# Optimization experiments

Hardware: AMD Instinct MI355X
Metric: run time of the kernel (lower is better)

## Reference

```python
import jax, jax.numpy as jnp
import numpy as np

N_NODES = 100000


def _segment_mean(h, src, dst, n_nodes):
    # copy_u: gather source features along edges, then mean-reduce per dst node
    msg = h[src]                                             # [E, D]
    s = jax.ops.segment_sum(msg, dst, num_segments=n_nodes)  # [N, D]
    cnt = jax.ops.segment_sum(jnp.ones((src.shape[0],), h.dtype), dst,
                              num_segments=n_nodes)          # [N]
    return s / jnp.maximum(cnt, 1.0)[:, None]


def setup_inputs() -> dict:
    key = jax.random.key(0)
    k1, k2, k3, k4, k5 = jax.random.split(key, 5)
    in_feats, n_hidden, n_classes = 128, 128, 64
    n_edges = 1600000
    features = jax.random.normal(k1, (N_NODES, in_feats), dtype=jnp.float32)
    W1 = jax.random.normal(k2, (in_feats, n_hidden), dtype=jnp.float32) * (1.0 / np.sqrt(in_feats))
    b1 = jnp.zeros((n_hidden,), jnp.float32)
    W2 = jax.random.normal(k3, (n_hidden, n_classes), dtype=jnp.float32) * (1.0 / np.sqrt(n_hidden))
    b2 = jnp.zeros((n_classes,), jnp.float32)
    src = jax.random.randint(k4, (n_edges,), 0, N_NODES, dtype=jnp.int64)
    dst = jax.random.randint(k5, (n_edges,), 0, N_NODES, dtype=jnp.int64)
    return {"features": features, "W1": W1, "b1": b1, "W2": W2, "b2": b2,
            "src": src, "dst": dst}


def reference(features, W1, b1, W2, b2, src, dst):
    # Layer 0: mean aggregation -> Linear -> relu  (dropout p=0.0 is identity)
    h = _segment_mean(features, src, dst, N_NODES)
    h = jax.nn.relu(h @ W1 + b1)
    # Layer 1: mean aggregation -> Linear (no activation on output layer)
    h = _segment_mean(h, src, dst, N_NODES)
    h = h @ W2 + b2
    return h
```

## Files before the change

kernel.cpp:

```cpp
#include <hip/hip_runtime.h>

#define N_NODES 100000
#define D 128
#define NE 1600000
#define C_OUT 64
#define NB 391
#define SENT 100000
#define P2B 256
#define P2E 6250
#define SEGSTRIDE 6400

typedef _Float16 half8 __attribute__((ext_vector_type(8)));
typedef float floatx4 __attribute__((ext_vector_type(4)));


__device__ inline half8 shfl_xor_h8(half8 v, int mask) {
    union { half8 h; int i[4]; } u;
    u.h = v;
    u.i[0] = __shfl_xor(u.i[0], mask);
    u.i[1] = __shfl_xor(u.i[1], mask);
    u.i[2] = __shfl_xor(u.i[2], mask);
    u.i[3] = __shfl_xor(u.i[3], mask);
    return u.h;
}

__device__ inline void pack_one(const float* W, _Float16* Wp, int tid, int N) {
    int l = tid & 63, p = tid >> 6;
    int nt = p >> 2, kc = p & 3;
    int quad = l >> 4, c = l & 15;
    int n = nt * 16 + c;
    half8 h;
    #pragma unroll
    for (int j = 0; j < 8; ++j) {
        int k = kc * 32 + quad * 8 + j;
        h[j] = (_Float16)W[k * N + n];
    }
    *(half8*)(Wp + (size_t)p * 512 + l * 8) = h;
}

__global__ __launch_bounds__(1024) void k1_p2_setup(const int* __restrict__ src,
                                                    const int* __restrict__ dst,
                                                    unsigned* __restrict__ gwords,
                                                    int* __restrict__ ofsg,
                                                    const float* __restrict__ W1,
                                                    const float* __restrict__ W2,
                                                    _Float16* __restrict__ wp1,
                                                    _Float16* __restrict__ wp2,
                                                    int* __restrict__ t1s,
                                                    int* __restrict__ t2s) {
    if (blockIdx.x >= P2B) {
        const int blk = blockIdx.x - P2B;
        const int t = threadIdx.x;
        if (t < 256) {
            if (blk < 8) {
                pack_one(W1, wp1, blk * 256 + t, 128);
            } else if (blk < 12) {
                pack_one(W2, wp2, (blk - 8) * 256 + t, 64);
            } else {
                if (t < 64) t1s[t] = 0;
                else if (t < 96) t2s[t - 64] = 0;
            }
        }
        return;
    }

    __shared__ unsigned ebuf[P2E];
    __shared__ int hist[NB];
    __shared__ int ofs[NB + 1];
    __shared__ int cur[NB];
    __shared__ int wsum[8];
    const int t = threadIdx.x;
    const int base = blockIdx.x * P2E;

    for (int i = t; i < NB; i += 1024) hist[i] = 0;
    __syncthreads();

    unsigned w[7];
    int bk[7];
    #pragma unroll
    for (int r = 0; r < 7; ++r) {
        const int j = r * 1024 + t;
        if (j < P2E) {
            const int e = base + j;
            const int d = dst[e];
            w[r] = ((unsigned)(d & 255) << 20) | (unsigned)src[e];
            bk[r] = d >> 8;
            atomicAdd(&hist[bk[r]], 1);
        } else {
            bk[r] = -1;
        }
    }
    __syncthreads();

    int v = 0, incl = 0;
    if (t < 512) { v = (t < NB) ? hist[t] : 0; incl = v; }
    #pragma unroll
    for (int d = 1; d < 64; d <<= 1) {
        int y = __shfl_up(incl, d);
        if ((t & 63) >= d) incl += y;
    }
    if (t < 512 && (t & 63) == 63) wsum[t >> 6] = incl;
    __syncthreads();
    if (t < NB) {
        int ex = incl - v;
        const int wv = t >> 6;
        for (int j = 0; j < wv; ++j) ex += wsum[j];
        ofs[t] = ex;
        cur[t] = ex;
    }
    if (t == 0) ofs[NB] = P2E;
    __syncthreads();

    #pragma unroll
    for (int r = 0; r < 7; ++r) {
        if (bk[r] >= 0) {
            const int slot = atomicAdd(&cur[bk[r]], 1);
            ebuf[slot] = w[r];
        }
    }
    __syncthreads();

    unsigned* gout = gwords + (size_t)blockIdx.x * SEGSTRIDE;
    for (int i = t; i < P2E; i += 1024) gout[i] = ebuf[i];
    int* oout = ofsg + blockIdx.x * (NB + 1);
    for (int i = t; i < NB + 1; i += 1024) oout[i] = ofs[i];
}

__global__ __launch_bounds__(256) void k2_p3_gemm1(const unsigned* __restrict__ gwords,
                                                   const int* __restrict__ ofsg,
                                                   int* __restrict__ ptrp,
                                                   int* __restrict__ pcnt,
                                                   float* __restrict__ inv,
                                                   int* __restrict__ csr,
                                                   const float* __restrict__ A,
                                                   const _Float16* __restrict__ Wp,
                                                   _Float16* __restrict__ outh) {
    __shared__ __align__(16) char smem[40960];
    const int t = threadIdx.x;

    if (blockIdx.x < NB) {
        unsigned* wbuf = (unsigned*)smem;
        int* sa   = (int*)(smem + 32768);
        int* so   = (int*)(smem + 33792);
        int* lcnt = (int*)(smem + 34816);
        int* lofs = (int*)(smem + 35840);
        int* ws4  = (int*)(smem + 36864);
        const int b = blockIdx.x;
        const int lane = t & 63, wave = t >> 6;

        const int* row = ofsg + t * (NB + 1);
        const int a0 = row[b];
        const int len = row[b + 1] - a0;
        sa[t] = a0;
        lcnt[t] = 0;
        int sv = a0;
        #pragma unroll
        for (int m2 = 1; m2 < 64; m2 <<= 1) sv += __shfl_xor(sv, m2);
        if (lane == 0) ws4[wave] = sv;
        __syncthreads();
        const int pad_base = (ws4[0] + ws4[1] + ws4[2] + ws4[3]) + 1792 * b;
        __syncthreads();

        int incl = len;
        #pragma unroll
        for (int d = 1; d < 64; d <<= 1) {
            int y = __shfl_up(incl, d);
            if (lane >= d) incl += y;
        }
        if (lane == 63) ws4[wave] = incl;
        __syncthreads();
        int off = incl - len;
        for (int j = 0; j < wave; ++j) off += ws4[j];
        so[t] = off;
        const int tot = min(ws4[0] + ws4[1] + ws4[2] + ws4[3], 8192);
        __syncthreads();

        {
            const int per = (tot + 255) >> 8;
            const int lo = t * per;
            const int hi = min(lo + per, tot);
            if (lo < hi) {
                int l = 0, r = P2B;
                while (r - l > 1) {
                    const int m = (l + r) >> 1;
                    if (so[m] <= lo) l = m; else r = m;
                }
                int sg = l;
                #pragma unroll 4
                for (int i = lo; i < hi; ++i) {
                    while (sg + 1 < P2B && so[sg + 1] <= i) ++sg;
                    const unsigned w = gwords[(size_t)sg * SEGSTRIDE + sa[sg] + (i - so[sg])];
                    wbuf[i] = w;
                    atomicAdd(&lcnt[(w >> 20) & 255], 1);
                }
            }
        }
        __syncthreads();

        const int v = lcnt[t];
        const int pc = (v + 7) & ~7;
        int incl2 = pc;
        #pragma unroll
        for (int d = 1; d < 64; d <<= 1) {
            int y = __shfl_up(incl2, d);
            if (lane >= d) incl2 += y;
        }
        __syncthreads();
        if (lane == 63) ws4[wave] = incl2;
        __syncthreads();
        int ex = incl2 - pc;
        for (int j = 0; j < wave; ++j) ex += ws4[j];

        const int node = b * 256 + t;
        if (node < N_NODES) {
            ptrp[node] = pad_base + ex;
            pcnt[node] = pc;
            inv[node] = 1.0f / fmaxf((float)v, 1.0f);
        }
        for (int j = v; j < pc; ++j) csr[pad_base + ex + j] = SENT;

        __syncthreads();
        lofs[t] = ex;
        __syncthreads();
        for (int i = t; i < tot; i += 256) {
            const unsigned w = wbuf[i];
            const int pos = atomicAdd(&lofs[(w >> 20) & 255], 1);
            csr[pad_base + pos] = (int)(w & 0xFFFFF);
        }
        return;
    }

    _Float16* Wl = (_Float16*)smem;
    _Float16* Al = (_Float16*)(smem + 32768);
    {
        const floatx4* s4 = (const floatx4*)Wp;
        floatx4* d4 = (floatx4*)Wl;
        #pragma unroll
        for (int i = 0; i < 8; ++i) d4[t + 256 * i] = s4[t + 256 * i];
    }
    const int lane = t & 63;
    const int wave = t >> 6;
    const int row0 = (blockIdx.x - NB) * 128;

    floatx4 acc[8][2];
    #pragma unroll
    for (int mt = 0; mt < 8; ++mt)
        #pragma unroll
        for (int nt = 0; nt < 2; ++nt) acc[mt][nt] = (floatx4)0.0f;

    for (int kc = 0; kc < 4; ++kc) {
        __syncthreads();
        #pragma unroll
        for (int rep = 0; rep < 2; ++rep) {
            int p = rep * 256 + t;
            int r = p >> 2, quad = p & 3;
            int row = row0 + r;
            if (row > N_NODES - 1) row = N_NODES - 1;
            const float4 x0 = *(const float4*)(A + (size_t)row * D + kc * 32 + quad * 8);
            const float4 x1 = *(const float4*)(A + (size_t)row * D + kc * 32 + quad * 8 + 4);
            half8 h;
            h[0] = (_Float16)x0.x; h[1] = (_Float16)x0.y;
            h[2] = (_Float16)x0.z; h[3] = (_Float16)x0.w;
            h[4] = (_Float16)x1.x; h[5] = (_Float16)x1.y;
            h[6] = (_Float16)x1.z; h[7] = (_Float16)x1.w;
            int mt = r >> 4, m = r & 15;
            *(half8*)(Al + mt * 512 + (quad * 16 + m) * 8) = h;
        }
        __syncthreads();
        const half8* Af = (const half8*)Al;
        const half8* Bf = (const half8*)Wl;
        half8 b0 = Bf[((wave * 2 + 0) * 4 + kc) * 64 + lane];
        half8 b1 = Bf[((wave * 2 + 1) * 4 + kc) * 64 + lane];
        #pragma unroll
        for (int mt = 0; mt < 8; ++mt) {
            half8 a = Af[mt * 64 + lane];
            acc[mt][0] = __builtin_amdgcn_mfma_f32_16x16x32_f16(a, b0, acc[mt][0], 0, 0, 0);
            acc[mt][1] = __builtin_amdgcn_mfma_f32_16x16x32_f16(a, b1, acc[mt][1], 0, 0, 0);
        }
    }

    const int quad = lane >> 4, cl = lane & 15;
    #pragma unroll
    for (int mt = 0; mt < 8; ++mt)
        #pragma unroll
        for (int nt = 0; nt < 2; ++nt) {
            int col = wave * 32 + nt * 16 + cl;
            #pragma unroll
            for (int i = 0; i < 4; ++i) {
                int row = row0 + mt * 16 + quad * 4 + i;
                if (row < N_NODES)
                    outh[(size_t)row * D + col] = (_Float16)acc[mt][nt][i];
            }
        }
}

__global__ __launch_bounds__(256) void kF_agg_gemm2(const _Float16* __restrict__ f,
                                                    const int* __restrict__ ptrp,
                                                    const int* __restrict__ pcnt,
                                                    const int* __restrict__ csr,
                                                    const float* __restrict__ inv,
                                                    const float* __restrict__ bias,
                                                    const _Float16* __restrict__ Wp,
                                                    _Float16* __restrict__ outh) {
    __shared__ __align__(16) _Float16 Wl[8192];
    __shared__ __align__(16) _Float16 h1t[16 * 136];
    const int t = threadIdx.x;
    {
        const floatx4* s4 = (const floatx4*)Wp;
        floatx4* d4 = (floatx4*)Wl;
        #pragma unroll
        for (int i = 0; i < 4; ++i) d4[t + 256 * i] = s4[t + 256 * i];
    }
    const int wave = t >> 6;
    const int lane = t & 63;
    const int q = lane & 15, hf = lane >> 4;
    const half8* f8 = (const half8*)f;

    for (int it = 0; it < 4; ++it) {
        const int r = wave * 4 + it;
        const int n = blockIdx.x * 16 + r;
        const int begin = ptrp[n];
        const int end = begin + pcnt[n];
        const float iv = inv[n];

        half8 acc0 = {0, 0, 0, 0, 0, 0, 0, 0};
        half8 acc1 = {0, 0, 0, 0, 0, 0, 0, 0};
        for (int base = begin; base < end; base += 64) {
            const int m = min(64, end - base);
            int edge = (lane < m) ? csr[base + lane] : SENT;
            int i = 0;
            for (; i + 16 <= m; i += 16) {
                int s0 = __shfl(edge, i + hf);
                int s1 = __shfl(edge, i + 4 + hf);
                int s2 = __shfl(edge, i + 8 + hf);
                int s3 = __shfl(edge, i + 12 + hf);
                half8 v0 = f8[(size_t)s0 * 16 + q];
                half8 v1 = f8[(size_t)s1 * 16 + q];
                half8 v2 = f8[(size_t)s2 * 16 + q];
                half8 v3 = f8[(size_t)s3 * 16 + q];
                acc0 += v0;
                acc1 += v1;
                acc0 += v2;
                acc1 += v3;
            }
            if (i < m) {
                int s0 = __shfl(edge, i + hf);
                int s1 = __shfl(edge, i + 4 + hf);
                half8 v0 = f8[(size_t)s0 * 16 + q];
                half8 v1 = f8[(size_t)s1 * 16 + q];
                acc0 += v0;
                acc1 += v1;
            }
        }
        acc0 += acc1;
        acc0 += shfl_xor_h8(acc0, 16);
        acc0 += shfl_xor_h8(acc0, 32);
        if (hf == 0) {
            const float4 b0 = ((const float4*)bias)[q * 2];
            const float4 b1v = ((const float4*)bias)[q * 2 + 1];
            half8 o;
            o[0] = (_Float16)fmaxf((float)acc0[0] * iv + b0.x, 0.f);
            o[1] = (_Float16)fmaxf((float)acc0[1] * iv + b0.y, 0.f);
            o[2] = (_Float16)fmaxf((float)acc0[2] * iv + b0.z, 0.f);
            o[3] = (_Float16)fmaxf((float)acc0[3] * iv + b0.w, 0.f);
            o[4] = (_Float16)fmaxf((float)acc0[4] * iv + b1v.x, 0.f);
            o[5] = (_Float16)fmaxf((float)acc0[5] * iv + b1v.y, 0.f);
            o[6] = (_Float16)fmaxf((float)acc0[6] * iv + b1v.z, 0.f);
            o[7] = (_Float16)fmaxf((float)acc0[7] * iv + b1v.w, 0.f);
            *(half8*)(h1t + r * 136 + q * 8) = o;
        }
    }
    __syncthreads();

    floatx4 acc = (floatx4)0.0f;
    #pragma unroll
    for (int kc = 0; kc < 4; ++kc) {
        half8 a = *(const half8*)(h1t + (lane & 15) * 136 + kc * 32 + (lane >> 4) * 8);
        half8 b = ((const half8*)Wl)[(wave * 4 + kc) * 64 + lane];
        acc = __builtin_amdgcn_mfma_f32_16x16x32_f16(a, b, acc, 0, 0, 0);
    }
    const int quad = lane >> 4, cl = lane & 15;
    const int col = wave * 16 + cl;
    #pragma unroll
    for (int i = 0; i < 4; ++i) {
        const int row = blockIdx.x * 16 + quad * 4 + i;
        outh[(size_t)row * C_OUT + col] = (_Float16)acc[i];
    }
}

__global__ __launch_bounds__(256) void kG_agg64(const _Float16* __restrict__ f,
                                                const int* __restrict__ ptrp,
                                                const int* __restrict__ pcnt,
                                                const int* __restrict__ csr,
                                                const float* __restrict__ inv,
                                                const float* __restrict__ bias,
                                                float* __restrict__ out) {
    const int wave = threadIdx.x >> 6;
    const int lane = threadIdx.x & 63;
    const int q = lane & 7, hf = lane >> 3;
    const int n = blockIdx.x * 4 + wave;
    const int begin = ptrp[n];
    const int end = begin + pcnt[n];
    const float iv = inv[n];
    const half8* f8 = (const half8*)f;

    half8 acc0 = {0, 0, 0, 0, 0, 0, 0, 0};
    half8 acc1 = {0, 0, 0, 0, 0, 0, 0, 0};
    for (int base = begin; base < end; base += 64) {
        const int m = min(64, end - base);
        int edge = (lane < m) ? csr[base + lane] : SENT;
        int i = 0;
        for (; i + 32 <= m; i += 32) {
            int s0 = __shfl(edge, i + hf);
            int s1 = __shfl(edge, i + 8 + hf);
            int s2 = __shfl(edge, i + 16 + hf);
            int s3 = __shfl(edge, i + 24 + hf);
            half8 v0 = f8[(size_t)s0 * 8 + q];
            half8 v1 = f8[(size_t)s1 * 8 + q];
            half8 v2 = f8[(size_t)s2 * 8 + q];
            half8 v3 = f8[(size_t)s3 * 8 + q];
            acc0 += v0;
            acc1 += v1;
            acc0 += v2;
            acc1 += v3;
        }
        if (i + 16 <= m) {
            int s0 = __shfl(edge, i + hf);
            int s1 = __shfl(edge, i + 8 + hf);
            half8 v0 = f8[(size_t)s0 * 8 + q];
            half8 v1 = f8[(size_t)s1 * 8 + q];
            acc0 += v0;
            acc1 += v1;
            i += 16;
        }
        if (i < m) {
            int s = __shfl(edge, i + hf);
            acc0 += f8[(size_t)s * 8 + q];
        }
    }
    acc0 += acc1;
    acc0 += shfl_xor_h8(acc0, 8);
    acc0 += shfl_xor_h8(acc0, 16);
    acc0 += shfl_xor_h8(acc0, 32);
    if (hf == 0) {
        const float4 b0 = ((const float4*)bias)[q * 2];
        const float4 b1 = ((const float4*)bias)[q * 2 + 1];
        float4 o0, o1;
        o0.x = (float)acc0[0] * iv + b0.x;
        o0.y = (float)acc0[1] * iv + b0.y;
        o0.z = (float)acc0[2] * iv + b0.z;
        o0.w = (float)acc0[3] * iv + b0.w;
        o1.x = (float)acc0[4] * iv + b1.x;
        o1.y = (float)acc0[5] * iv + b1.y;
        o1.z = (float)acc0[6] * iv + b1.z;
        o1.w = (float)acc0[7] * iv + b1.w;
        ((float4*)out)[(size_t)n * 16 + q * 2] = o0;
        ((float4*)out)[(size_t)n * 16 + q * 2 + 1] = o1;
    }
}

extern "C" void kernel_launch(void* const* d_in, const int* in_sizes, int n_in,
                              void* d_out, int out_size, void* d_ws, size_t ws_size,
                              hipStream_t stream) {
    const float* features = (const float*)d_in[0];
    const float* W1 = (const float*)d_in[1];
    const float* b1 = (const float*)d_in[2];
    const float* W2 = (const float*)d_in[3];
    const float* b2 = (const float*)d_in[4];
    const int* src = (const int*)d_in[5];
    const int* dst = (const int*)d_in[6];
    float* out = (float*)d_out;

    char* ws = (char*)d_ws;
    int*      ofsg  = (int*)(ws + 512L * 4);
    int*      ptrp  = (int*)(ws + 125952L * 4);
    int*      pcnt  = (int*)(ws + 225952L * 4);
    float*    inv   = (float*)(ws + 325952L * 4);
    int*      csr   = (int*)(ws + 425952L * 4);
    unsigned* gwords= (unsigned*)(ws + 2825952L * 4);
    _Float16* wp1   = (_Float16*)(ws + 4464352L * 4);
    _Float16* wp2   = (_Float16*)(ws + 4472544L * 4);
    _Float16* t1h   = (_Float16*)(ws + 4476640L * 4);
    _Float16* t2h   = (_Float16*)(ws + 17276704L * 4);

    k1_p2_setup<<<P2B + 13, 1024, 0, stream>>>(src, dst, gwords, ofsg, W1, W2, wp1, wp2,
                                               (int*)(t1h + (size_t)SENT * 128),
                                               (int*)(t2h + (size_t)SENT * 64));
    k2_p3_gemm1<<<NB + 782, 256, 0, stream>>>(gwords, ofsg, ptrp, pcnt, inv, csr,
                                              features, wp1, t1h);
    kF_agg_gemm2<<<N_NODES / 16, 256, 0, stream>>>(t1h, ptrp, pcnt, csr, inv, b1, wp2, t2h);
    kG_agg64<<<N_NODES / 4, 256, 0, stream>>>(t2h, ptrp, pcnt, csr, inv, b2, out);
}
```

Before: 228.8 us.

## Move GEMM1 into the first kernel alongside edge bucketing, packing W1 per block

The dense features@W1 GEMM no longer shares a launch with CSR phase 3; it now runs in the first kernel, concurrently with the per-chunk edge bucketing (phase 2). Phase 3 becomes its own small kernel. Each GEMM block packs W1 into fp16 in LDS directly instead of reading a pre-packed copy, and the bucketing blocks are reshaped from 1024 to 256 threads. The goal is to hide the GEMM behind the atomics-bound bucketing pass, at the cost of redundant W1 conversion in every GEMM block and lower per-block parallelism in bucketing.

```diff
diff --git a/kernel.cpp b/kernel.cpp
--- a/kernel.cpp
+++ b/kernel.cpp
@@ -9,6 +9,7 @@
 #define P2B 256
 #define P2E 6250
 #define SEGSTRIDE 6400
+#define GOFF 261
 
 typedef _Float16 half8 __attribute__((ext_vector_type(8)));
 typedef float floatx4 __attribute__((ext_vector_type(4)));
@@ -38,209 +39,110 @@
     *(half8*)(Wp + (size_t)p * 512 + l * 8) = h;
 }
 
-__global__ __launch_bounds__(1024) void k1_p2_setup(const int* __restrict__ src,
-                                                    const int* __restrict__ dst,
-                                                    unsigned* __restrict__ gwords,
-                                                    int* __restrict__ ofsg,
-                                                    const float* __restrict__ W1,
-                                                    const float* __restrict__ W2,
-                                                    _Float16* __restrict__ wp1,
-                                                    _Float16* __restrict__ wp2,
-                                                    int* __restrict__ t1s,
-                                                    int* __restrict__ t2s) {
-    if (blockIdx.x >= P2B) {
-        const int blk = blockIdx.x - P2B;
-        const int t = threadIdx.x;
-        if (t < 256) {
-            if (blk < 8) {
-                pack_one(W1, wp1, blk * 256 + t, 128);
-            } else if (blk < 12) {
-                pack_one(W2, wp2, (blk - 8) * 256 + t, 64);
-            } else {
-                if (t < 64) t1s[t] = 0;
-                else if (t < 96) t2s[t - 64] = 0;
-            }
-        }
-        return;
-    }
-
-    __shared__ unsigned ebuf[P2E];
-    __shared__ int hist[NB];
-    __shared__ int ofs[NB + 1];
-    __shared__ int cur[NB];
-    __shared__ int wsum[8];
+__global__ __launch_bounds__(256) void k1_all(const int* __restrict__ src,
+                                              const int* __restrict__ dst,
+                                              unsigned* __restrict__ gwords,
+                                              int* __restrict__ ofsg,
+                                              const float* __restrict__ W1,
+                                              const float* __restrict__ W2,
+                                              _Float16* __restrict__ wp2,
+                                              int* __restrict__ t1s,
+                                              int* __restrict__ t2s,
+                                              const float* __restrict__ A,
+                                              _Float16* __restrict__ outh) {
+    __shared__ __align__(16) char smem[40960];
     const int t = threadIdx.x;
-    const int base = blockIdx.x * P2E;
-
-    for (int i = t; i < NB; i += 1024) hist[i] = 0;
-    __syncthreads();
-
-    unsigned w[7];
-    int bk[7];
-    #pragma unroll
-    for (int r = 0; r < 7; ++r) {
-        const int j = r * 1024 + t;
-        if (j < P2E) {
+
+    if (blockIdx.x < P2B) {
+        unsigned* ebuf = (unsigned*)smem;
+        int* hist = (int*)(smem + 25088);
+        int* ofs  = (int*)(smem + 27136);
+        int* cur  = (int*)(smem + 28736);
+        int* ws4  = (int*)(smem + 30336);
+        const int base = blockIdx.x * P2E;
+        const int lane = t & 63, wave = t >> 6;
+
+        hist[t] = 0;
+        hist[t + 256] = 0;
+        __syncthreads();
+
+        for (int j = t; j < P2E; j += 256)
+            atomicAdd(&hist[dst[base + j] >> 8], 1);
+        __syncthreads();
+
+        int v0 = hist[t], i0 = v0;
+        #pragma unroll
+        for (int d = 1; d < 64; d <<= 1) {
+            int y = __shfl_up(i0, d);
+            if (lane >= d) i0 += y;
+        }
+        if (lane == 63) ws4[wave] = i0;
+        __syncthreads();
+        int ex0 = i0 - v0;
+        for (int j = 0; j < wave; ++j) ex0 += ws4[j];
+        const int tot0 = ws4[0] + ws4[1] + ws4[2] + ws4[3];
+        __syncthreads();
+        int v1 = hist[256 + t], i1 = v1;
+        #pragma unroll
+        for (int d = 1; d < 64; d <<= 1) {
+            int y = __shfl_up(i1, d);
+            if (lane >= d) i1 += y;
+        }
+        if (lane == 63) ws4[wave] = i1;
+        __syncthreads();
+        int ex1 = i1 - v1 + tot0;
+        for (int j = 0; j < wave; ++j) ex1 += ws4[j];
+        ofs[t] = ex0;
+        cur[t] = ex0;
+        if (256 + t < NB) { ofs[256 + t] = ex1; cur[256 + t] = ex1; }
+        if (t == 0) ofs[NB] = P2E;
+        __syncthreads();
+
+        for (int j = t; j < P2E; j += 256) {
             const int e = base + j;
             const int d = dst[e];
-            w[r] = ((unsigned)(d & 255) << 20) | (unsigned)src[e];
-            bk[r] = d >> 8;
-            atomicAdd(&hist[bk[r]], 1);
+            const unsigned w = ((unsigned)(d & 255) << 20) | (unsigned)src[e];
+            const int slot = atomicAdd(&cur[d >> 8], 1);
+            ebuf[slot] = w;
+        }
+        __syncthreads();
+
+        unsigned* gout = gwords + (size_t)blockIdx.x * SEGSTRIDE;
+        for (int i = t; i < P2E; i += 256) gout[i] = ebuf[i];
+        int* oout = ofsg + blockIdx.x * (NB + 1);
+        for (int i = t; i < NB + 1; i += 256) oout[i] = ofs[i];
+        return;
+    }
+
+    if (blockIdx.x < GOFF) {
+        const int blk = blockIdx.x - P2B;
+        if (blk < 4) {
+            pack_one(W2, wp2, blk * 256 + t, 64);
         } else {
-            bk[r] = -1;
-        }
-    }
-    __syncthreads();
-
-    int v = 0, incl = 0;
-    if (t < 512) { v = (t < NB) ? hist[t] : 0; incl = v; }
-    #pragma unroll
-    for (int d = 1; d < 64; d <<= 1) {
-        int y = __shfl_up(incl, d);
-        if ((t & 63) >= d) incl += y;
-    }
-    if (t < 512 && (t & 63) == 63) wsum[t >> 6] = incl;
-    __syncthreads();
-    if (t < NB) {
-        int ex = incl - v;
-        const int wv = t >> 6;
-        for (int j = 0; j < wv; ++j) ex += wsum[j];
-        ofs[t] = ex;
-        cur[t] = ex;
-    }
-    if (t == 0) ofs[NB] = P2E;
-    __syncthreads();
-
-    #pragma unroll
-    for (int r = 0; r < 7; ++r) {
-        if (bk[r] >= 0) {
-            const int slot = atomicAdd(&cur[bk[r]], 1);
-            ebuf[slot] = w[r];
-        }
-    }
-    __syncthreads();
-
-    unsigned* gout = gwords + (size_t)blockIdx.x * SEGSTRIDE;
-    for (int i = t; i < P2E; i += 1024) gout[i] = ebuf[i];
-    int* oout = ofsg + blockIdx.x * (NB + 1);
-    for (int i = t; i < NB + 1; i += 1024) oout[i] = ofs[i];
-}
-
-__global__ __launch_bounds__(256) void k2_p3_gemm1(const unsigned* __restrict__ gwords,
-                                                   const int* __restrict__ ofsg,
-                                                   int* __restrict__ ptrp,
-                                                   int* __restrict__ pcnt,
-                                                   float* __restrict__ inv,
-                                                   int* __restrict__ csr,
-                                                   const float* __restrict__ A,
-                                                   const _Float16* __restrict__ Wp,
-                                                   _Float16* __restrict__ outh) {
-    __shared__ __align__(16) char smem[40960];
-    const int t = threadIdx.x;
-
-    if (blockIdx.x < NB) {
-        unsigned* wbuf = (unsigned*)smem;
-        int* sa   = (int*)(smem + 32768);
-        int* so   = (int*)(smem + 33792);
-        int* lcnt = (int*)(smem + 34816);
-        int* lofs = (int*)(smem + 35840);
-        int* ws4  = (int*)(smem + 36864);
-        const int b = blockIdx.x;
-        const int lane = t & 63, wave = t >> 6;
-
-        const int* row = ofsg + t * (NB + 1);
-        const int a0 = row[b];
-        const int len = row[b + 1] - a0;
-        sa[t] = a0;
-        lcnt[t] = 0;
-        int sv = a0;
-        #pragma unroll
-        for (int m2 = 1; m2 < 64; m2 <<= 1) sv += __shfl_xor(sv, m2);
-        if (lane == 0) ws4[wave] = sv;
-        __syncthreads();
-        const int pad_base = (ws4[0] + ws4[1] + ws4[2] + ws4[3]) + 1792 * b;
-        __syncthreads();
-
-        int incl = len;
-        #pragma unroll
-        for (int d = 1; d < 64; d <<= 1) {
-            int y = __shfl_up(incl, d);
-            if (lane >= d) incl += y;
-        }
-        if (lane == 63) ws4[wave] = incl;
-        __syncthreads();
-        int off = incl - len;
-        for (int j = 0; j < wave; ++j) off += ws4[j];
-        so[t] = off;
-        const int tot = min(ws4[0] + ws4[1] + ws4[2] + ws4[3], 8192);
-        __syncthreads();
-
-        {
-            const int per = (tot + 255) >> 8;
-            const int lo = t * per;
-            const int hi = min(lo + per, tot);
-            if (lo < hi) {
-                int l = 0, r = P2B;
-                while (r - l > 1) {
-                    const int m = (l + r) >> 1;
-                    if (so[m] <= lo) l = m; else r = m;
-                }
-                int sg = l;
-                #pragma unroll 4
-                for (int i = lo; i < hi; ++i) {
-                    while (sg + 1 < P2B && so[sg + 1] <= i) ++sg;
-                    const unsigned w = gwords[(size_t)sg * SEGSTRIDE + sa[sg] + (i - so[sg])];
-                    wbuf[i] = w;
-                    atomicAdd(&lcnt[(w >> 20) & 255], 1);
-                }
-            }
-        }
-        __syncthreads();
-
-        const int v = lcnt[t];
-        const int pc = (v + 7) & ~7;
-        int incl2 = pc;
-        #pragma unroll
-        for (int d = 1; d < 64; d <<= 1) {
-            int y = __shfl_up(incl2, d);
-            if (lane >= d) incl2 += y;
-        }
-        __syncthreads();
-        if (lane == 63) ws4[wave] = incl2;
-        __syncthreads();
-        int ex = incl2 - pc;
-        for (int j = 0; j < wave; ++j) ex += ws4[j];
-
-        const int node = b * 256 + t;
-        if (node < N_NODES) {
-            ptrp[node] = pad_base + ex;
-            pcnt[node] = pc;
-            inv[node] = 1.0f / fmaxf((float)v, 1.0f);
-        }
-        for (int j = v; j < pc; ++j) csr[pad_base + ex + j] = SENT;
-
-        __syncthreads();
-        lofs[t] = ex;
-        __syncthreads();
-        for (int i = t; i < tot; i += 256) {
-            const unsigned w = wbuf[i];
-            const int pos = atomicAdd(&lofs[(w >> 20) & 255], 1);
-            csr[pad_base + pos] = (int)(w & 0xFFFFF);
+            if (t < 64) t1s[t] = 0;
+            else if (t < 96) t2s[t - 64] = 0;
         }
         return;
     }
 
     _Float16* Wl = (_Float16*)smem;
     _Float16* Al = (_Float16*)(smem + 32768);
-    {
-        const floatx4* s4 = (const floatx4*)Wp;
-        floatx4* d4 = (floatx4*)Wl;
-        #pragma unroll
-        for (int i = 0; i < 8; ++i) d4[t + 256 * i] = s4[t + 256 * i];
+    #pragma unroll
+    for (int rep = 0; rep < 8; ++rep) {
+        const int tid = rep * 256 + t;
+        const int l = tid & 63, p = tid >> 6;
+        const int nt = p >> 2, kc2 = p & 3;
+        const int quad = l >> 4, c = l & 15;
+        const int n = nt * 16 + c;
+        half8 h;
+        #pragma unroll
+        for (int j = 0; j < 8; ++j)
+            h[j] = (_Float16)W1[(kc2 * 32 + quad * 8 + j) * 128 + n];
+        *(half8*)(Wl + (size_t)p * 512 + l * 8) = h;
     }
     const int lane = t & 63;
     const int wave = t >> 6;
-    const int row0 = (blockIdx.x - NB) * 128;
+    const int row0 = (blockIdx.x - GOFF) * 128;
 
     floatx4 acc[8][2];
     #pragma unroll
@@ -292,6 +194,104 @@
                     outh[(size_t)row * D + col] = (_Float16)acc[mt][nt][i];
             }
         }
+}
+
+__global__ __launch_bounds__(256) void k2_p3(const unsigned* __restrict__ gwords,
+                                             const int* __restrict__ ofsg,
+                                             int* __restrict__ ptrp,
+                                             int* __restrict__ pcnt,
+                                             float* __restrict__ inv,
+                                             int* __restrict__ csr) {
+    __shared__ __align__(16) char smem[40960];
+    unsigned* wbuf = (unsigned*)smem;
+    int* sa   = (int*)(smem + 32768);
+    int* so   = (int*)(smem + 33792);
+    int* lcnt = (int*)(smem + 34816);
+    int* lofs = (int*)(smem + 35840);
+    int* ws4  = (int*)(smem + 36864);
+    const int b = blockIdx.x;
+    const int t = threadIdx.x;
+    const int lane = t & 63, wave = t >> 6;
+
+    const int* row = ofsg + t * (NB + 1);
+    const int a0 = row[b];
+    const int len = row[b + 1] - a0;
+    sa[t] = a0;
+    lcnt[t] = 0;
+    int sv = a0;
+    #pragma unroll
+    for (int m2 = 1; m2 < 64; m2 <<= 1) sv += __shfl_xor(sv, m2);
+    if (lane == 0) ws4[wave] = sv;
+    __syncthreads();
+    const int pad_base = (ws4[0] + ws4[1] + ws4[2] + ws4[3]) + 1792 * b;
+    __syncthreads();
+
+    int incl = len;
+    #pragma unroll
+    for (int d = 1; d < 64; d <<= 1) {
+        int y = __shfl_up(incl, d);
+        if (lane >= d) incl += y;
+    }
+    if (lane == 63) ws4[wave] = incl;
+    __syncthreads();
+    int off = incl - len;
+    for (int j = 0; j < wave; ++j) off += ws4[j];
+    so[t] = off;
+    const int tot = min(ws4[0] + ws4[1] + ws4[2] + ws4[3], 8192);
+    __syncthreads();
+
+    {
+        const int per = (tot + 255) >> 8;
+        const int lo = t * per;
+        const int hi = min(lo + per, tot);
+        if (lo < hi) {
+            int l = 0, r = P2B;
+            while (r - l > 1) {
+                const int m = (l + r) >> 1;
+                if (so[m] <= lo) l = m; else r = m;
+            }
+            int sg = l;
+            #pragma unroll 4
+            for (int i = lo; i < hi; ++i) {
+                while (sg + 1 < P2B && so[sg + 1] <= i) ++sg;
+                const unsigned w = gwords[(size_t)sg * SEGSTRIDE + sa[sg] + (i - so[sg])];
+                wbuf[i] = w;
+                atomicAdd(&lcnt[(w >> 20) & 255], 1);
+            }
+        }
+    }
+    __syncthreads();
+
+    const int v = lcnt[t];
+    const int pc = (v + 7) & ~7;
+    int incl2 = pc;
+    #pragma unroll
+    for (int d = 1; d < 64; d <<= 1) {
+        int y = __shfl_up(incl2, d);
+        if (lane >= d) incl2 += y;
+    }
+    __syncthreads();
+    if (lane == 63) ws4[wave] = incl2;
+    __syncthreads();
+    int ex = incl2 - pc;
+    for (int j = 0; j < wave; ++j) ex += ws4[j];
+
+    const int node = b * 256 + t;
+    if (node < N_NODES) {
+        ptrp[node] = pad_base + ex;
+        pcnt[node] = pc;
+        inv[node] = 1.0f / fmaxf((float)v, 1.0f);
+    }
+    for (int j = v; j < pc; ++j) csr[pad_base + ex + j] = SENT;
+
+    __syncthreads();
+    lofs[t] = ex;
+    __syncthreads();
+    for (int i = t; i < tot; i += 256) {
+        const unsigned w = wbuf[i];
+        const int pos = atomicAdd(&lofs[(w >> 20) & 255], 1);
+        csr[pad_base + pos] = (int)(w & 0xFFFFF);
+    }
 }
 
 __global__ __launch_bounds__(256) void kF_agg_gemm2(const _Float16* __restrict__ f,
@@ -478,16 +478,15 @@
     float*    inv   = (float*)(ws + 325952L * 4);
     int*      csr   = (int*)(ws + 425952L * 4);
     unsigned* gwords= (unsigned*)(ws + 2825952L * 4);
-    _Float16* wp1   = (_Float16*)(ws + 4464352L * 4);
     _Float16* wp2   = (_Float16*)(ws + 4472544L * 4);
     _Float16* t1h   = (_Float16*)(ws + 4476640L * 4);
     _Float16* t2h   = (_Float16*)(ws + 17276704L * 4);
 
-    k1_p2_setup<<<P2B + 13, 1024, 0, stream>>>(src, dst, gwords, ofsg, W1, W2, wp1, wp2,
-                                               (int*)(t1h + (size_t)SENT * 128),
-                                               (int*)(t2h + (size_t)SENT * 64));
-    k2_p3_gemm1<<<NB + 782, 256, 0, stream>>>(gwords, ofsg, ptrp, pcnt, inv, csr,
-                                              features, wp1, t1h);
+    k1_all<<<GOFF + 782, 256, 0, stream>>>(src, dst, gwords, ofsg, W1, W2, wp2,
+                                           (int*)(t1h + (size_t)SENT * 128),
+                                           (int*)(t2h + (size_t)SENT * 64),
+                                           features, t1h);
+    k2_p3<<<NB, 256, 0, stream>>>(gwords, ofsg, ptrp, pcnt, inv, csr);
     kF_agg_gemm2<<<N_NODES / 16, 256, 0, stream>>>(t1h, ptrp, pcnt, csr, inv, b1, wp2, t2h);
     kG_agg64<<<N_NODES / 4, 256, 0, stream>>>(t2h, ptrp, pcnt, csr, inv, b2, out);
 }
```

Measured after the change: 243.6 us. 6.5% more time.
